# Kernel tuning notes

Hardware: AMD Instinct MI355X
Metric: run time of the kernel (lower is better)

## Reference

```python
import jax, jax.numpy as jnp
import numpy as np

H, D_MODEL, LEN_Q, LEN_K, D_K, D_V = 16, 1024, 2048, 2048, 64, 64
BATCH = 4
SCALE = 1.0 / np.sqrt(float(D_K))


def setup_inputs() -> dict:
    key = jax.random.key(0)
    ks = jax.random.split(key, 10)
    inp = {
        "Q": jax.random.normal(ks[0], (BATCH, LEN_Q, D_MODEL), dtype=jnp.float32),
        "K": jax.random.normal(ks[1], (BATCH, LEN_K, D_MODEL), dtype=jnp.float32),
        "V": jax.random.normal(ks[2], (BATCH, LEN_K, D_MODEL), dtype=jnp.float32),
        "mask": jax.random.randint(ks[3], (BATCH, LEN_K), 0, 2, dtype=jnp.int32),
        # Linear params (torch Linear: y = x @ W.T + b); store W as [in, out].
        "Wq": jax.random.normal(ks[4], (D_MODEL, H * D_K), dtype=jnp.float32) * (1.0 / np.sqrt(D_MODEL)),
        "bq": jnp.zeros((H * D_K,), dtype=jnp.float32),
        "Wk": jax.random.normal(ks[5], (D_MODEL, H * D_K), dtype=jnp.float32) * (1.0 / np.sqrt(D_MODEL)),
        "bk": jnp.zeros((H * D_K,), dtype=jnp.float32),
        "Wv": jax.random.normal(ks[6], (D_MODEL, H * D_V), dtype=jnp.float32) * (1.0 / np.sqrt(D_MODEL)),
        "bv": jnp.zeros((H * D_V,), dtype=jnp.float32),
    }
    return inp


def reference(Q, K, V, mask, Wq, bq, Wk, bk, Wv, bv):
    B = Q.shape[0]
    # Projections -> [B, S, H, d]
    q = (Q @ Wq + bq).reshape(B, LEN_Q, H, D_K)
    k = (K @ Wk + bk).reshape(B, LEN_K, H, D_K)
    v = (V @ Wv + bv).reshape(B, LEN_K, H, D_V)
    # Scores: [B, H, len_q, len_k]
    scores = jnp.einsum("bqhd,bkhd->bhqk", q, k) * SCALE
    # Key-padding mask broadcast over heads and queries
    scores = jnp.where(mask[:, None, None, :] == 0, jnp.float32(-1e9), scores)
    alpha = jax.nn.softmax(scores, axis=-1)
    out = jnp.einsum("bhqk,bkhd->bqhd", alpha, v)  # [B, len_q, H, d_v]
    return out.reshape(B, LEN_Q, H * D_V)
```

## Files before the change

kernel.cpp:

```cpp
#include <hip/hip_runtime.h>

#define NH 16
#define DM 1024
#define SQ 2048
#define BT 4

typedef __attribute__((ext_vector_type(8))) short bf16x8;
typedef __attribute__((ext_vector_type(4))) short sh4;
typedef __attribute__((ext_vector_type(4))) float f4;
typedef __attribute__((ext_vector_type(4))) float fv4;
typedef __attribute__((ext_vector_type(4))) unsigned uv4;
typedef unsigned short u16;

#define M2BIAS 23.083120654f
#define SCALE2 0.18033688f

__device__ __forceinline__ u16 f2bf(float f) {
    union { float f; unsigned u; } v; v.f = f;
    unsigned r = v.u + 0x7FFFu + ((v.u >> 16) & 1u);
    return (u16)(r >> 16);
}

__device__ __forceinline__ float fast_exp2(float x) {
#if __has_builtin(__builtin_amdgcn_exp2f)
    return __builtin_amdgcn_exp2f(x);
#else
    return exp2f(x);
#endif
}

__device__ __forceinline__ int prem(int s) {
    return (s & ~31) | ((s & 4) << 2) | ((s >> 1) & 12) | (s & 3);
}

#define GLD16(gp, lp) __builtin_amdgcn_global_load_lds( \
    (const __attribute__((address_space(1))) void*)(gp), \
    (__attribute__((address_space(3))) void*)(lp), 16, 0, 0)

__global__ __launch_bounds__(256) void cvt_wT3(const float* __restrict__ W0, const float* __restrict__ W1,
                                               const float* __restrict__ W2, u16* __restrict__ Wt) {
    __shared__ float t[64][65];
    const float* Wsrc = blockIdx.z == 0 ? W0 : (blockIdx.z == 1 ? W1 : W2);
    u16* dst = Wt + (size_t)blockIdx.z * DM * DM;
    int r0 = blockIdx.x * 64, c0 = blockIdx.y * 64;
    #pragma unroll
    for (int i = 0; i < 16; ++i) {
        int idx = i * 256 + threadIdx.x;
        int r = idx >> 6, c = idx & 63;
        t[r][c] = Wsrc[(size_t)(r0 + r) * DM + c0 + c];
    }
    __syncthreads();
    #pragma unroll
    for (int i = 0; i < 16; ++i) {
        int idx = i * 256 + threadIdx.x;
        int n = idx >> 6, k = idx & 63;
        dst[(size_t)(c0 + n) * DM + r0 + k] = f2bf(t[k][n]);
    }
}

__global__ __launch_bounds__(256) void mk_mbias(const int* __restrict__ mask, float* __restrict__ mb) {
    int i = blockIdx.x * 256 + threadIdx.x;
    mb[prem(i)] = mask[i] ? -M2BIAS : -__builtin_inff();
}

__global__ __launch_bounds__(256, 3) void gemm3(const float* __restrict__ Qf, const float* __restrict__ Kf,
                                                const float* __restrict__ Vf, const u16* __restrict__ Wt3,
                                                const float* __restrict__ bq, const float* __restrict__ bk,
                                                const float* __restrict__ bv, u16* __restrict__ out3) {
    __shared__ u16 As[128 * 64];
    __shared__ u16 Bs[128 * 64];
    int z = blockIdx.z;
    const float* Af = z == 0 ? Qf : (z == 1 ? Kf : Vf);
    const float* bias = z == 0 ? bq : (z == 1 ? bk : bv);
    int vmode = z == 0 ? 0 : (z == 1 ? 2 : 1);
    const u16* Bg = Wt3 + (size_t)z * DM * DM + (size_t)blockIdx.y * 128 * DM;
    u16* outp = out3 + (size_t)z * 8388608u;

    int tid = threadIdx.x;
    int w = tid >> 6, lane = tid & 63, quad = lane >> 4, l16 = lane & 15;
    int wm = w >> 1, wn = w & 1;
    int r8 = lane >> 3, cg = (lane & 7) ^ r8;

    int arow0 = w * 32 + (lane >> 4);
    int acol = (lane & 15) * 4;
    const float* Ag = Af + (size_t)(blockIdx.x * 128 + arow0) * DM + acol;
    int ach = (lane & 15) >> 1, asub = lane & 1;

    f4 acc[4][4];
    #pragma unroll
    for (int mt = 0; mt < 4; ++mt)
        #pragma unroll
        for (int nt = 0; nt < 4; ++nt) acc[mt][nt] = f4{0.f, 0.f, 0.f, 0.f};

    fv4 ar[8];
    #pragma unroll
    for (int j = 0; j < 8; ++j) ar[j] = *(const fv4*)(Ag + (size_t)j * 4 * DM);

    for (int kt = 0; kt < 16; ++kt) {
        int kofs = kt * 64 + cg * 8;
        #pragma unroll
        for (int c = 0; c < 4; ++c) {
            int rbase = w * 32 + c * 8;
            GLD16(Bg + (size_t)(rbase + r8) * DM + kofs, &Bs[rbase * 64]);
        }
        #pragma unroll
        for (int j = 0; j < 8; ++j) {
            unsigned lo, hi;
            asm("v_cvt_pk_bf16_f32 %0, %1, %2" : "=v"(lo) : "v"(ar[j][0]), "v"(ar[j][1]));
            asm("v_cvt_pk_bf16_f32 %0, %1, %2" : "=v"(hi) : "v"(ar[j][2]), "v"(ar[j][3]));
            int row = arow0 + j * 4;
            uint2 pk; pk.x = lo; pk.y = hi;
            *(uint2*)&As[row * 64 + (ach ^ (row & 7)) * 8 + asub * 4] = pk;
        }
        if (kt + 1 < 16) {
            const float* src = Ag + (kt + 1) * 64;
            #pragma unroll
            for (int j = 0; j < 8; ++j) ar[j] = *(const fv4*)(src + (size_t)j * 4 * DM);
        }
        __syncthreads();
        #pragma unroll
        for (int ks = 0; ks < 2; ++ks) {
            bf16x8 afr[4], bfr[4];
            #pragma unroll
            for (int mt = 0; mt < 4; ++mt) {
                int row = wm * 64 + mt * 16 + l16;
                int ch = (ks * 4 + quad) ^ (row & 7);
                afr[mt] = *(const bf16x8*)&As[row * 64 + ch * 8];
            }
            #pragma unroll
            for (int nt = 0; nt < 4; ++nt) {
                int row = wn * 64 + nt * 16 + l16;
                int ch = (ks * 4 + quad) ^ (row & 7);
                bfr[nt] = *(const bf16x8*)&Bs[row * 64 + ch * 8];
            }
            #pragma unroll
            for (int mt = 0; mt < 4; ++mt)
                #pragma unroll
                for (int nt = 0; nt < 4; ++nt)
                    acc[mt][nt] = __builtin_amdgcn_mfma_f32_16x16x32_bf16(afr[mt], bfr[nt], acc[mt][nt], 0, 0, 0);
        }
        __syncthreads();
    }

    #pragma unroll
    for (int nt = 0; nt < 4; ++nt) {
        int ncol = blockIdx.y * 128 + wn * 64 + nt * 16 + l16;
        float bn = bias[ncol];
        int h = ncol >> 6, d = ncol & 63;
        #pragma unroll
        for (int mt = 0; mt < 4; ++mt) {
            int mbase = blockIdx.x * 128 + wm * 64 + mt * 16 + quad * 4;
            int bidx = mbase >> 11, s0 = mbase & 2047;
            if (vmode == 1) {
                sh4 pk;
                #pragma unroll
                for (int reg = 0; reg < 4; ++reg) pk[reg] = (short)f2bf(acc[mt][nt][reg] + bn);
                *(sh4*)&outp[(((size_t)bidx * NH + h) * 64 + d) * SQ + s0] = pk;
            } else {
                int sp = (vmode == 2) ? prem(s0) : s0;
                size_t base = ((size_t)bidx * NH + h) * SQ;
                #pragma unroll
                for (int reg = 0; reg < 4; ++reg)
                    outp[(base + sp + reg) * 64 + d] = f2bf(acc[mt][nt][reg] + bn);
            }
        }
    }
}

__global__ __launch_bounds__(256, 4) void attn(const u16* __restrict__ qw, const u16* __restrict__ kw,
                                               const u16* __restrict__ vtw, const float* __restrict__ mbias,
                                               float* __restrict__ outp) {
    __shared__ u16 Ks[2][64 * 64];
    __shared__ u16 Vs[2][64 * 64];
    int tid = threadIdx.x;
    int w = tid >> 6, lane = tid & 63, quad = lane >> 4, l16 = lane & 15;
    int r8 = lane >> 3, sl = lane & 7;
    int bh = blockIdx.x, b = bh >> 4;
    int h = bh & 15;
    int qbase = blockIdx.y * 128 + w * 32;
    const u16* qp = qw + (size_t)bh * SQ * 64;
    const u16* kp = kw + (size_t)bh * SQ * 64;
    const u16* vp = vtw + (size_t)bh * 64 * SQ;
    const float* mbp = mbias + b * SQ;

    bf16x8 aq[2][2];
    #pragma unroll
    for (int mt = 0; mt < 2; ++mt)
        #pragma unroll
        for (int ks = 0; ks < 2; ++ks)
            aq[mt][ks] = *(const bf16x8*)&qp[(size_t)(qbase + mt * 16 + l16) * 64 + ks * 32 + quad * 8];

    f4 o[2][4];
    float lrow[2] = {0.f, 0.f};
    #pragma unroll
    for (int mt = 0; mt < 2; ++mt)
        #pragma unroll
        for (int nt = 0; nt < 4; ++nt) o[mt][nt] = f4{0.f, 0.f, 0.f, 0.f};

    auto stage = [&](int buf, int k0) {
        #pragma unroll
        for (int j = 0; j < 2; ++j) {
            int row = w * 16 + j * 8 + r8;
            int gsl = sl ^ (row & 7);
            GLD16(kp + (size_t)(k0 + row) * 64 + gsl * 8, &Ks[buf][(w * 16 + j * 8) * 64]);
            GLD16(vp + (size_t)row * SQ + k0 + gsl * 8, &Vs[buf][(w * 16 + j * 8) * 64]);
        }
    };

    stage(0, 0);
    for (int kb = 0; kb < 32; ++kb) {
        int buf = kb & 1;
        int k0 = kb * 64;
        __syncthreads();
        fv4 bias4[4];
        #pragma unroll
        for (int kt = 0; kt < 4; ++kt)
            bias4[kt] = *(const fv4*)&mbp[k0 + kt * 16 + quad * 4];
        if (kb + 1 < 32) stage(buf ^ 1, k0 + 64);

        bf16x8 bk[4][2];
        #pragma unroll
        for (int kt = 0; kt < 4; ++kt)
            #pragma unroll
            for (int ks = 0; ks < 2; ++ks) {
                int r = kt * 16 + l16;
                int slot = (ks * 4 + quad) ^ (r & 7);
                bk[kt][ks] = *(const bf16x8*)&Ks[buf][r * 64 + slot * 8];
            }
        f4 S[4][2];
        #pragma unroll
        for (int kt = 0; kt < 4; ++kt)
            #pragma unroll
            for (int mt = 0; mt < 2; ++mt) {
                f4 s = f4{0.f, 0.f, 0.f, 0.f};
                s = __builtin_amdgcn_mfma_f32_16x16x32_bf16(bk[kt][0], aq[mt][0], s, 0, 0, 0);
                s = __builtin_amdgcn_mfma_f32_16x16x32_bf16(bk[kt][1], aq[mt][1], s, 0, 0, 0);
                S[kt][mt] = s;
            }
        bf16x8 pa8[2][2];
        #pragma unroll
        for (int g = 0; g < 2; ++g)
            #pragma unroll
            for (int mt = 0; mt < 2; ++mt) {
                f4 se = S[2 * g][mt], so = S[2 * g + 1][mt];
                float p0 = fast_exp2(se[0] * SCALE2 + bias4[2 * g][0]);
                float p1 = fast_exp2(se[1] * SCALE2 + bias4[2 * g][1]);
                float p2 = fast_exp2(se[2] * SCALE2 + bias4[2 * g][2]);
                float p3 = fast_exp2(se[3] * SCALE2 + bias4[2 * g][3]);
                float q0 = fast_exp2(so[0] * SCALE2 + bias4[2 * g + 1][0]);
                float q1 = fast_exp2(so[1] * SCALE2 + bias4[2 * g + 1][1]);
                float q2 = fast_exp2(so[2] * SCALE2 + bias4[2 * g + 1][2]);
                float q3 = fast_exp2(so[3] * SCALE2 + bias4[2 * g + 1][3]);
                lrow[mt] += ((p0 + p1) + (p2 + p3)) + ((q0 + q1) + (q2 + q3));
                uv4 wv;
                wv[0] = (__float_as_uint(p1) & 0xFFFF0000u) | (__float_as_uint(p0) >> 16);
                wv[1] = (__float_as_uint(p3) & 0xFFFF0000u) | (__float_as_uint(p2) >> 16);
                wv[2] = (__float_as_uint(q1) & 0xFFFF0000u) | (__float_as_uint(q0) >> 16);
                wv[3] = (__float_as_uint(q3) & 0xFFFF0000u) | (__float_as_uint(q2) >> 16);
                pa8[g][mt] = __builtin_bit_cast(bf16x8, wv);
            }
        #pragma unroll
        for (int g = 0; g < 2; ++g) {
            bf16x8 bv8[4];
            #pragma unroll
            for (int nt = 0; nt < 4; ++nt) {
                int row = nt * 16 + l16;
                int ch = (g * 4 + quad) ^ (row & 7);
                bv8[nt] = *(const bf16x8*)&Vs[buf][row * 64 + ch * 8];
            }
            #pragma unroll
            for (int mt = 0; mt < 2; ++mt)
                #pragma unroll
                for (int nt = 0; nt < 4; ++nt)
                    o[mt][nt] = __builtin_amdgcn_mfma_f32_16x16x32_bf16(pa8[g][mt], bv8[nt], o[mt][nt], 0, 0, 0);
        }
    }

    #pragma unroll
    for (int mt = 0; mt < 2; ++mt) {
        float v = lrow[mt];
        v += __shfl_xor(v, 16);
        v += __shfl_xor(v, 32);
        #pragma unroll
        for (int reg = 0; reg < 4; ++reg) {
            float inv = 1.f / __shfl(v, quad * 4 + reg);
            int row = qbase + mt * 16 + quad * 4 + reg;
            size_t obase = ((size_t)b * SQ + row) * DM + h * 64;
            #pragma unroll
            for (int nt = 0; nt < 4; ++nt)
                outp[obase + nt * 16 + l16] = o[mt][nt][reg] * inv;
        }
    }
}

extern "C" void kernel_launch(void* const* d_in, const int* in_sizes, int n_in,
                              void* d_out, int out_size, void* d_ws, size_t ws_size,
                              hipStream_t stream) {
    (void)in_sizes; (void)n_in; (void)out_size; (void)ws_size;
    const float* Q  = (const float*)d_in[0];
    const float* K  = (const float*)d_in[1];
    const float* V  = (const float*)d_in[2];
    const int* mask = (const int*)d_in[3];
    const float* Wq = (const float*)d_in[4];
    const float* bq = (const float*)d_in[5];
    const float* Wk = (const float*)d_in[6];
    const float* bk = (const float*)d_in[7];
    const float* Wv = (const float*)d_in[8];
    const float* bv = (const float*)d_in[9];
    float* out = (float*)d_out;
    char* ws = (char*)d_ws;
    u16* q_ws  = (u16*)(ws);
    u16* k_ws  = (u16*)(ws + (size_t)16 * 1024 * 1024);
    u16* v_ws  = (u16*)(ws + (size_t)32 * 1024 * 1024);
    u16* wbuf3 = (u16*)(ws + (size_t)48 * 1024 * 1024);
    float* mb  = (float*)(ws + (size_t)54 * 1024 * 1024);

    cvt_wT3<<<dim3(16, 16, 3), 256, 0, stream>>>(Wq, Wk, Wv, wbuf3);
    mk_mbias<<<32, 256, 0, stream>>>(mask, mb);
    gemm3<<<dim3(64, 8, 3), 256, 0, stream>>>(Q, K, V, wbuf3, bq, bk, bv, q_ws);
    attn<<<dim3(64, 16), 256, 0, stream>>>(q_ws, k_ws, v_ws, mb, out);
}
```

Baseline: 321.8 us.

## Double-buffer weight tiles and prefetch A two steps ahead in projection GEMM

Restructures the QKV projection GEMM main loop into a software pipeline: the bf16 weight tile goes into a double-buffered LDS array and is issued one k-step ahead, and fp32 activation rows are loaded two k-steps ahead into two alternating register sets. Explicit vmcnt waits replace the full wait before the barrier, so only the loads needed for the current step must land. This aims to hide global-load latency behind MFMA work, at the cost of extra LDS (16KB more) and more VGPRs, which may reduce occupancy under the 3-block launch bound.

```diff
diff --git a/kernel.cpp b/kernel.cpp
--- a/kernel.cpp
+++ b/kernel.cpp
@@ -68,7 +68,7 @@
                                                 const float* __restrict__ bq, const float* __restrict__ bk,
                                                 const float* __restrict__ bv, u16* __restrict__ out3) {
     __shared__ u16 As[128 * 64];
-    __shared__ u16 Bs[128 * 64];
+    __shared__ u16 Bs[2][128 * 64];
     int z = blockIdx.z;
     const float* Af = z == 0 ? Qf : (z == 1 ? Kf : Vf);
     const float* bias = z == 0 ? bq : (z == 1 ? bk : bv);
@@ -92,55 +92,86 @@
         #pragma unroll
         for (int nt = 0; nt < 4; ++nt) acc[mt][nt] = f4{0.f, 0.f, 0.f, 0.f};
 
-    fv4 ar[8];
-    #pragma unroll
-    for (int j = 0; j < 8; ++j) ar[j] = *(const fv4*)(Ag + (size_t)j * 4 * DM);
-
-    for (int kt = 0; kt < 16; ++kt) {
+    fv4 arA[8], arB[8];
+    auto stageB = [&](int buf, int kt) {
         int kofs = kt * 64 + cg * 8;
         #pragma unroll
         for (int c = 0; c < 4; ++c) {
             int rbase = w * 32 + c * 8;
-            GLD16(Bg + (size_t)(rbase + r8) * DM + kofs, &Bs[rbase * 64]);
-        }
-        #pragma unroll
-        for (int j = 0; j < 8; ++j) {
-            unsigned lo, hi;
-            asm("v_cvt_pk_bf16_f32 %0, %1, %2" : "=v"(lo) : "v"(ar[j][0]), "v"(ar[j][1]));
-            asm("v_cvt_pk_bf16_f32 %0, %1, %2" : "=v"(hi) : "v"(ar[j][2]), "v"(ar[j][3]));
-            int row = arow0 + j * 4;
-            uint2 pk; pk.x = lo; pk.y = hi;
-            *(uint2*)&As[row * 64 + (ach ^ (row & 7)) * 8 + asub * 4] = pk;
-        }
-        if (kt + 1 < 16) {
-            const float* src = Ag + (kt + 1) * 64;
-            #pragma unroll
-            for (int j = 0; j < 8; ++j) ar[j] = *(const fv4*)(src + (size_t)j * 4 * DM);
-        }
-        __syncthreads();
-        #pragma unroll
-        for (int ks = 0; ks < 2; ++ks) {
-            bf16x8 afr[4], bfr[4];
-            #pragma unroll
-            for (int mt = 0; mt < 4; ++mt) {
-                int row = wm * 64 + mt * 16 + l16;
-                int ch = (ks * 4 + quad) ^ (row & 7);
-                afr[mt] = *(const bf16x8*)&As[row * 64 + ch * 8];
-            }
-            #pragma unroll
-            for (int nt = 0; nt < 4; ++nt) {
-                int row = wn * 64 + nt * 16 + l16;
-                int ch = (ks * 4 + quad) ^ (row & 7);
-                bfr[nt] = *(const bf16x8*)&Bs[row * 64 + ch * 8];
-            }
-            #pragma unroll
-            for (int mt = 0; mt < 4; ++mt)
-                #pragma unroll
-                for (int nt = 0; nt < 4; ++nt)
-                    acc[mt][nt] = __builtin_amdgcn_mfma_f32_16x16x32_bf16(afr[mt], bfr[nt], acc[mt][nt], 0, 0, 0);
-        }
-        __syncthreads();
-    }
+            GLD16(Bg + (size_t)(rbase + r8) * DM + kofs, &Bs[buf][rbase * 64]);
+        }
+    };
+
+#define LOADA(ar, kt) do { \
+        const float* _src = Ag + (kt) * 64; \
+        _Pragma("unroll") \
+        for (int j = 0; j < 8; ++j) (ar)[j] = *(const fv4*)(_src + (size_t)j * 4 * DM); \
+    } while (0)
+
+#define CVTA(ar) do { \
+        _Pragma("unroll") \
+        for (int j = 0; j < 8; ++j) { \
+            unsigned lo, hi; \
+            asm("v_cvt_pk_bf16_f32 %0, %1, %2" : "=v"(lo) : "v"((ar)[j][0]), "v"((ar)[j][1])); \
+            asm("v_cvt_pk_bf16_f32 %0, %1, %2" : "=v"(hi) : "v"((ar)[j][2]), "v"((ar)[j][3])); \
+            int row = arow0 + j * 4; \
+            uint2 pk; pk.x = lo; pk.y = hi; \
+            *(uint2*)&As[row * 64 + (ach ^ (row & 7)) * 8 + asub * 4] = pk; \
+        } \
+    } while (0)
+
+#define MFMAPHASE(bufidx) do { \
+        _Pragma("unroll") \
+        for (int ks = 0; ks < 2; ++ks) { \
+            bf16x8 afr[4], bfr[4]; \
+            _Pragma("unroll") \
+            for (int mt = 0; mt < 4; ++mt) { \
+                int row = wm * 64 + mt * 16 + l16; \
+                int ch = (ks * 4 + quad) ^ (row & 7); \
+                afr[mt] = *(const bf16x8*)&As[row * 64 + ch * 8]; \
+            } \
+            _Pragma("unroll") \
+            for (int nt = 0; nt < 4; ++nt) { \
+                int row = wn * 64 + nt * 16 + l16; \
+                int ch = (ks * 4 + quad) ^ (row & 7); \
+                bfr[nt] = *(const bf16x8*)&Bs[bufidx][row * 64 + ch * 8]; \
+            } \
+            _Pragma("unroll") \
+            for (int mt = 0; mt < 4; ++mt) \
+                _Pragma("unroll") \
+                for (int nt = 0; nt < 4; ++nt) \
+                    acc[mt][nt] = __builtin_amdgcn_mfma_f32_16x16x32_bf16(afr[mt], bfr[nt], acc[mt][nt], 0, 0, 0); \
+        } \
+    } while (0)
+
+#define SUBITER(k, ar, VM) do { \
+        if ((k) + 1 < 16) stageB(((k) + 1) & 1, (k) + 1); \
+        CVTA(ar); \
+        if ((k) + 2 < 16) LOADA(ar, (k) + 2); \
+        asm volatile("s_waitcnt vmcnt(" #VM ") lgkmcnt(0)" ::: "memory"); \
+        __builtin_amdgcn_s_barrier(); \
+        asm volatile("" ::: "memory"); \
+        MFMAPHASE((k) & 1); \
+        asm volatile("" ::: "memory"); \
+        __builtin_amdgcn_s_barrier(); \
+        asm volatile("" ::: "memory"); \
+    } while (0)
+
+    stageB(0, 0);
+    LOADA(arA, 0);
+    LOADA(arB, 1);
+
+    for (int k = 0; k < 14; k += 2) {
+        SUBITER(k, arA, 20);
+        SUBITER(k + 1, arB, 20);
+    }
+    SUBITER(14, arA, 12);
+    SUBITER(15, arB, 0);
+
+#undef SUBITER
+#undef MFMAPHASE
+#undef CVTA
+#undef LOADA
 
     #pragma unroll
     for (int nt = 0; nt < 4; ++nt) {
```

Result: slower. 478.4 us (+48.7%).
